# Kernel optimization log

Measured on AMD Instinct MI355X. Metric: run time of the kernel, lower is better.

Reference implementation:

```python
import jax, jax.numpy as jnp
import numpy as np

EMBED = 1024
HEADS = 16
HEAD_DIM = EMBED // HEADS
B, N = 2, 2048


def setup_inputs() -> dict:
    key = jax.random.key(0)
    ks = jax.random.split(key, 7)
    s = 1.0 / np.sqrt(EMBED)
    x = jax.random.normal(ks[0], (B, N, EMBED), dtype=jnp.float32)
    # causal mask: 1 where attention allowed, 0 elsewhere (masked_fill on mask==0)
    mask = jnp.tril(jnp.ones((N, N), dtype=jnp.int32))[None, None, :, :]
    Wq = jax.random.uniform(ks[1], (EMBED, EMBED), jnp.float32, -s, s)
    Wk = jax.random.uniform(ks[2], (EMBED, EMBED), jnp.float32, -s, s)
    Wv = jax.random.uniform(ks[3], (EMBED, EMBED), jnp.float32, -s, s)
    Wo = jax.random.uniform(ks[4], (EMBED, EMBED), jnp.float32, -s, s)
    bo = jax.random.uniform(ks[5], (EMBED,), jnp.float32, -s, s)
    return {"x": x, "mask": mask, "Wq": Wq, "Wk": Wk, "Wv": Wv, "Wo": Wo, "bo": bo}


def reference(x, mask, Wq, Wk, Wv, Wo, bo):
    Bx, Nx, D = x.shape
    # torch nn.Linear: y = x @ W.T
    q = (x @ Wq.T).reshape(Bx, Nx, HEADS, HEAD_DIM).transpose(0, 2, 1, 3)
    k = (x @ Wk.T).reshape(Bx, Nx, HEADS, HEAD_DIM).transpose(0, 2, 1, 3)
    v = (x @ Wv.T).reshape(Bx, Nx, HEADS, HEAD_DIM).transpose(0, 2, 1, 3)
    score = jnp.einsum('bhqd,bhkd->bhqk', q, k) / np.sqrt(HEAD_DIM).astype(np.float32)
    score = jnp.where(mask == 0, -jnp.inf, score)
    probs = jax.nn.softmax(score, axis=-1)
    out = jnp.einsum('bhqk,bhkd->bhqd', probs, v)  # [B,H,N,hd]
    out = out.transpose(0, 2, 1, 3).reshape(Bx, Nx, D)
    return out @ Wo.T + bo
```

## Files before the change

kernel.cpp:

```cpp
#include <hip/hip_runtime.h>
#include <hip/hip_bf16.h>

#define B_  2
#define N_  2048
#define E_  1024
#define H_  16
#define HD_ 64
#define M_  (B_*N_)
#define RSZ ((size_t)M_ * E_)

typedef short bf16x8 __attribute__((ext_vector_type(8)));
typedef float f32x4 __attribute__((ext_vector_type(4)));
typedef unsigned short u16x8 __attribute__((ext_vector_type(8)));

#define AS1 __attribute__((address_space(1)))
#define AS3 __attribute__((address_space(3)))

__device__ __forceinline__ unsigned short f2bfu(float f) {
    __hip_bfloat16 h = __float2bfloat16(f);
    return *reinterpret_cast<unsigned short*>(&h);
}
__device__ __forceinline__ unsigned int cvtpk(float lo, float hi) {
    unsigned int r;
    asm("v_cvt_pk_bf16_f32 %0, %1, %2" : "=v"(r) : "v"(lo), "v"(hi));
    return r;
}
#define MFMA16(a,b,c) __builtin_amdgcn_mfma_f32_16x16x32_bf16((a),(b),(c),0,0,0)

__device__ __forceinline__ void gl_lds16(const void* g, void* l) {
    __builtin_amdgcn_global_load_lds((const AS1 void*)g, (AS3 void*)l, 16, 0, 0);
}

__global__ __launch_bounds__(256) void fconv_all_kernel(
    const float* __restrict__ x,
    const float* __restrict__ Wq, const float* __restrict__ Wk,
    const float* __restrict__ Wv, const float* __restrict__ Wo,
    unsigned short* __restrict__ xbf, unsigned short* __restrict__ wbf)
{
    const int bid = blockIdx.x;
    const float* src;
    unsigned short* dst;
    int off;
    if (bid < 2048) {
        src = x; dst = xbf; off = bid * 2048 + threadIdx.x * 8;
    } else {
        const int z = (bid - 2048) >> 9;
        src = (z == 0) ? Wq : (z == 1 ? Wk : (z == 2 ? Wv : Wo));
        dst = wbf + (size_t)z * E_ * E_;
        off = ((bid - 2048) & 511) * 2048 + threadIdx.x * 8;
    }
    const float4 a = *reinterpret_cast<const float4*>(src + off);
    const float4 b = *reinterpret_cast<const float4*>(src + off + 4);
    u16x8 v;
    v[0]=f2bfu(a.x); v[1]=f2bfu(a.y); v[2]=f2bfu(a.z); v[3]=f2bfu(a.w);
    v[4]=f2bfu(b.x); v[5]=f2bfu(b.y); v[6]=f2bfu(b.z); v[7]=f2bfu(b.w);
    *reinterpret_cast<u16x8*>(dst + off) = v;
}

__global__ __launch_bounds__(256) void fconv_kernel(
    const float* __restrict__ src, unsigned short* __restrict__ dst)
{
    const int i0 = (blockIdx.x * 256 + threadIdx.x) * 8;
    const float4 a = *reinterpret_cast<const float4*>(src + i0);
    const float4 b = *reinterpret_cast<const float4*>(src + i0 + 4);
    u16x8 v;
    v[0]=f2bfu(a.x); v[1]=f2bfu(a.y); v[2]=f2bfu(a.z); v[3]=f2bfu(a.w);
    v[4]=f2bfu(b.x); v[5]=f2bfu(b.y); v[6]=f2bfu(b.z); v[7]=f2bfu(b.w);
    *reinterpret_cast<u16x8*>(dst + i0) = v;
}

__global__ __launch_bounds__(256) void qkv_fused_kernel(
    const unsigned short* __restrict__ xbf, const unsigned short* __restrict__ wbf,
    unsigned short* __restrict__ qkv)
{
    const int m0 = blockIdx.x * 64;
    const int n0 = blockIdx.y * 128;
    __shared__ unsigned short ldsA[64*64];
    __shared__ unsigned short ldsB[3][128*64];
    const int t = threadIdx.x;
    const int lane = t & 63;
    const int w = t >> 6, wr = w >> 1, wc = w & 1;
    const int fr = lane & 15, fq = lane >> 4;
    const int subrow = lane >> 3;
    const int csw = ((lane & 7) ^ subrow) * 8;
    const int rcol = ((fq * 8) ^ ((fr & 7) * 8));
    f32x4 acc[3][2][4] = {};

    for (int kt = 0; kt < 16; ++kt) {
        const int k0 = kt * 64;
        __syncthreads();
        #pragma unroll
        for (int i = 0; i < 14; ++i) {
            const int c = w * 14 + i;
            if (c < 8) {
                const int row = c * 8 + subrow;
                gl_lds16(xbf + (size_t)(m0 + row) * E_ + k0 + csw, &ldsA[c * 512]);
            } else {
                const int cc = c - 8;
                const int zb = cc >> 4, bc = cc & 15;
                const int row = bc * 8 + subrow;
                gl_lds16(wbf + (size_t)zb * E_ * E_ + (size_t)(n0 + row) * E_ + k0 + csw,
                         &ldsB[zb][bc * 512]);
            }
        }
        __syncthreads();
        #pragma unroll
        for (int ks = 0; ks < 2; ++ks) {
            bf16x8 af[2];
            #pragma unroll
            for (int mf = 0; mf < 2; ++mf)
                af[mf] = *(const bf16x8*)&ldsA[(wr*32 + mf*16 + fr)*64 + (rcol ^ (ks*32))];
            #pragma unroll
            for (int zb = 0; zb < 3; ++zb) {
                bf16x8 bfv[4];
                #pragma unroll
                for (int nf = 0; nf < 4; ++nf)
                    bfv[nf] = *(const bf16x8*)&ldsB[zb][(wc*64 + nf*16 + fr)*64 + (rcol ^ (ks*32))];
                #pragma unroll
                for (int mf = 0; mf < 2; ++mf)
                    #pragma unroll
                    for (int nf = 0; nf < 4; ++nf)
                        acc[zb][mf][nf] = MFMA16(af[mf], bfv[nf], acc[zb][mf][nf]);
            }
        }
    }

    #pragma unroll
    for (int zb = 0; zb < 3; ++zb) {
        unsigned short* __restrict__ out = qkv + (size_t)zb * RSZ;
        const float scale = (zb == 0) ? 0.125f : 1.0f;
        #pragma unroll
        for (int mf = 0; mf < 2; ++mf) {
            #pragma unroll
            for (int r = 0; r < 4; ++r) {
                const int m = m0 + wr*32 + mf*16 + fq*4 + r;
                const int b = m >> 11, npos = m & (N_ - 1);
                #pragma unroll
                for (int nf = 0; nf < 4; ++nf) {
                    const int n = n0 + wc*64 + nf*16 + fr;
                    const int h = n >> 6, d = n & 63;
                    const unsigned short val = f2bfu(acc[zb][mf][nf][r] * scale);
                    if (zb == 2)
                        out[(((size_t)(b*H_ + h))*HD_ + d)*N_ + npos] = val;
                    else
                        out[(((size_t)(b*H_ + h))*N_ + npos)*HD_ + d] = val;
                }
            }
        }
    }
}

__global__ __launch_bounds__(256) void qkv_f32_kernel(
    const float* __restrict__ x, const unsigned short* __restrict__ wbf,
    unsigned short* __restrict__ qkv)
{
    const int z = blockIdx.z;
    const unsigned short* __restrict__ W = wbf + (size_t)z * E_ * E_;
    unsigned short* __restrict__ out = qkv + (size_t)z * RSZ;
    const int m0 = blockIdx.x * 128;
    const int n0 = blockIdx.y * 128;
    __shared__ unsigned short As[128][72];
    __shared__ unsigned short Bs[128][72];
    const int t = threadIdx.x;
    const int lane = t & 63;
    const int w = t >> 6, wr = w >> 1, wc = w & 1;
    const int fr = lane & 15, fq = lane >> 4;
    const int srow = t >> 1, scol = (t & 1) * 32;
    f32x4 acc[4][4] = {};

    const float* arow = x + (size_t)(m0 + srow) * E_ + scol;
    const unsigned short* brow = W + (size_t)(n0 + srow) * E_ + scol;

    float4 a4[8];
    u16x8 b8[4];
    #pragma unroll
    for (int i = 0; i < 8; ++i) a4[i] = reinterpret_cast<const float4*>(arow)[i];
    #pragma unroll
    for (int i = 0; i < 4; ++i) b8[i] = reinterpret_cast<const u16x8*>(brow)[i];

    for (int k0 = 0; k0 < E_; k0 += 64) {
        __syncthreads();
        #pragma unroll
        for (int j = 0; j < 4; ++j) {
            u16x8 va;
            va[0]=f2bfu(a4[2*j].x); va[1]=f2bfu(a4[2*j].y); va[2]=f2bfu(a4[2*j].z); va[3]=f2bfu(a4[2*j].w);
            va[4]=f2bfu(a4[2*j+1].x); va[5]=f2bfu(a4[2*j+1].y); va[6]=f2bfu(a4[2*j+1].z); va[7]=f2bfu(a4[2*j+1].w);
            *reinterpret_cast<u16x8*>(&As[srow][scol + 8*j]) = va;
            *reinterpret_cast<u16x8*>(&Bs[srow][scol + 8*j]) = b8[j];
        }
        __syncthreads();
        if (k0 + 64 < E_) {
            #pragma unroll
            for (int i = 0; i < 8; ++i)
                a4[i] = reinterpret_cast<const float4*>(arow + k0 + 64)[i];
            #pragma unroll
            for (int i = 0; i < 4; ++i)
                b8[i] = reinterpret_cast<const u16x8*>(brow + k0 + 64)[i];
        }
        #pragma unroll
        for (int ks = 0; ks < 2; ++ks) {
            bf16x8 af[4], bfv[4];
            #pragma unroll
            for (int mf = 0; mf < 4; ++mf)
                af[mf] = *reinterpret_cast<const bf16x8*>(&As[wr*64 + mf*16 + fr][ks*32 + fq*8]);
            #pragma unroll
            for (int nf = 0; nf < 4; ++nf)
                bfv[nf] = *reinterpret_cast<const bf16x8*>(&Bs[wc*64 + nf*16 + fr][ks*32 + fq*8]);
            #pragma unroll
            for (int mf = 0; mf < 4; ++mf)
                #pragma unroll
                for (int nf = 0; nf < 4; ++nf)
                    acc[mf][nf] = MFMA16(af[mf], bfv[nf], acc[mf][nf]);
        }
    }

    const float scale = (z == 0) ? 0.125f : 1.0f;
    #pragma unroll
    for (int mf = 0; mf < 4; ++mf) {
        #pragma unroll
        for (int r = 0; r < 4; ++r) {
            const int m = m0 + wr*64 + mf*16 + fq*4 + r;
            const int b = m >> 11, npos = m & (N_ - 1);
            #pragma unroll
            for (int nf = 0; nf < 4; ++nf) {
                const int n = n0 + wc*64 + nf*16 + fr;
                const int h = n >> 6, d = n & 63;
                const unsigned short val = f2bfu(acc[mf][nf][r] * scale);
                if (z == 2)
                    out[(((size_t)(b*H_ + h))*HD_ + d)*N_ + npos] = val;
                else
                    out[(((size_t)(b*H_ + h))*N_ + npos)*HD_ + d] = val;
            }
        }
    }
}

__global__ __launch_bounds__(512) void attn_mfma_kernel(
    const unsigned short* __restrict__ qkv, unsigned short* __restrict__ attn_out)
{
    const int bh = blockIdx.x;
    const int xp = blockIdx.y;
    const unsigned short* Qp  = qkv + (size_t)bh * N_ * HD_;
    const unsigned short* Kp  = qkv + RSZ + (size_t)bh * N_ * HD_;
    const unsigned short* Vtp = qkv + 2*RSZ + (size_t)bh * N_ * HD_;
    __shared__ unsigned short Ks[128][72], Vt[64][136];
    const int t = threadIdx.x;
    const int lane = t & 63, w = t >> 6;
    const int fr = lane & 15, fq = lane >> 4;
    const int srK = t >> 2, scK = (t & 3) * 16;
    const int srV = t >> 3, scV = (t & 7) * 16;
    const int qbase = (w < 4) ? ((31 - xp) * 64 + w * 16)
                              : (xp * 64 + (w - 4) * 16);
    const int KT = (33 - xp) >> 1;
    const int ql = qbase + fr;
    const int lane_b0 = (2 * (fq & 1)) * 16 + fr;
    const int lane_b1 = lane_b0 + 16;
    const bool hi_sel = (fq >> 1) != 0;

    bf16x8 qfr[2];
    #pragma unroll
    for (int ks = 0; ks < 2; ++ks)
        qfr[ks] = *reinterpret_cast<const bf16x8*>(
            Qp + (size_t)ql * HD_ + ks*32 + fq*8);

    float m_run = -1e30f, l_run = 0.f;
    f32x4 o[4] = {};

    u16x8 kra = *reinterpret_cast<const u16x8*>(Kp + (size_t)srK * HD_ + scK);
    u16x8 krb = *reinterpret_cast<const u16x8*>(Kp + (size_t)srK * HD_ + scK + 8);
    u16x8 vra = *reinterpret_cast<const u16x8*>(Vtp + (size_t)srV * N_ + scV);
    u16x8 vrb = *reinterpret_cast<const u16x8*>(Vtp + (size_t)srV * N_ + scV + 8);

    for (int kt = 0; kt < KT; ++kt) {
        const int k0 = kt * 128;
        __syncthreads();
        *reinterpret_cast<u16x8*>(&Ks[srK][scK])     = kra;
        *reinterpret_cast<u16x8*>(&Ks[srK][scK + 8]) = krb;
        *reinterpret_cast<u16x8*>(&Vt[srV][scV])     = vra;
        *reinterpret_cast<u16x8*>(&Vt[srV][scV + 8]) = vrb;
        __syncthreads();
        if (kt + 1 < KT) {
            const int kn = k0 + 128;
            kra = *reinterpret_cast<const u16x8*>(Kp + (size_t)(kn + srK) * HD_ + scK);
            krb = *reinterpret_cast<const u16x8*>(Kp + (size_t)(kn + srK) * HD_ + scK + 8);
            vra = *reinterpret_cast<const u16x8*>(Vtp + (size_t)srV * N_ + kn + scV);
            vrb = *reinterpret_cast<const u16x8*>(Vtp + (size_t)srV * N_ + kn + scV + 8);
        }
        if (k0 > qbase + 15) continue;

        f32x4 s[8] = {};
        __builtin_amdgcn_s_setprio(1);
        #pragma unroll
        for (int ks = 0; ks < 2; ++ks) {
            #pragma unroll
            for (int nf = 0; nf < 8; ++nf) {
                bf16x8 bk = *reinterpret_cast<const bf16x8*>(&Ks[nf*16 + fr][ks*32 + fq*8]);
                s[nf] = MFMA16(bk, qfr[ks], s[nf]);
            }
        }
        __builtin_amdgcn_s_setprio(0);

        if (k0 + 127 > qbase) {
            #pragma unroll
            for (int nf = 0; nf < 8; ++nf)
                #pragma unroll
                for (int r = 0; r < 4; ++r)
                    if (k0 + nf*16 + fq*4 + r > ql) s[nf][r] = -1e30f;
        }

        float pm = -1e30f;
        #pragma unroll
        for (int nf = 0; nf < 8; ++nf)
            pm = fmaxf(pm, fmaxf(fmaxf(s[nf][0], s[nf][1]),
                                 fmaxf(s[nf][2], s[nf][3])));
        pm = fmaxf(pm, __shfl_xor(pm, 16));
        pm = fmaxf(pm, __shfl_xor(pm, 32));

        const bool need = __any(pm > m_run + 8.f);
        float scl = 1.f;
        if (need) {
            const float mnew = fmaxf(m_run, pm);
            scl = __expf(m_run - mnew);
            m_run = mnew;
        }

        float rs = 0.f;
        unsigned int u[8][2];
        #pragma unroll
        for (int nf = 0; nf < 8; ++nf) {
            const float p0 = __expf(s[nf][0] - m_run);
            const float p1 = __expf(s[nf][1] - m_run);
            const float p2 = __expf(s[nf][2] - m_run);
            const float p3 = __expf(s[nf][3] - m_run);
            rs += (p0 + p1) + (p2 + p3);
            u[nf][0] = cvtpk(p0, p1);
            u[nf][1] = cvtpk(p2, p3);
        }
        {
            float v = rs;
            v += __shfl_xor(v, 16);
            v += __shfl_xor(v, 32);
            l_run = l_run * scl + v;
        }
        if (need) {
            #pragma unroll
            for (int df = 0; df < 4; ++df)
                #pragma unroll
                for (int r = 0; r < 4; ++r)
                    o[df][r] *= scl;
        }

        bf16x8 pb[4];
        #pragma unroll
        for (int kk = 0; kk < 4; ++kk) {
            const unsigned int t00 = __shfl(u[2*kk+0][0], lane_b0);
            const unsigned int t01 = __shfl(u[2*kk+0][1], lane_b0);
            const unsigned int t02 = __shfl(u[2*kk+0][0], lane_b1);
            const unsigned int t03 = __shfl(u[2*kk+0][1], lane_b1);
            const unsigned int t10 = __shfl(u[2*kk+1][0], lane_b0);
            const unsigned int t11 = __shfl(u[2*kk+1][1], lane_b0);
            const unsigned int t12 = __shfl(u[2*kk+1][0], lane_b1);
            const unsigned int t13 = __shfl(u[2*kk+1][1], lane_b1);
            union { unsigned int wd[4]; bf16x8 v; } pu;
            pu.wd[0] = hi_sel ? t10 : t00;
            pu.wd[1] = hi_sel ? t11 : t01;
            pu.wd[2] = hi_sel ? t12 : t02;
            pu.wd[3] = hi_sel ? t13 : t03;
            pb[kk] = pu.v;
        }

        __builtin_amdgcn_s_setprio(1);
        #pragma unroll
        for (int kk = 0; kk < 4; ++kk) {
            bf16x8 bv[4];
            #pragma unroll
            for (int df = 0; df < 4; ++df)
                bv[df] = *reinterpret_cast<const bf16x8*>(&Vt[df*16 + fr][kk*32 + fq*8]);
            #pragma unroll
            for (int df = 0; df < 4; ++df)
                o[df] = MFMA16(bv[df], pb[kk], o[df]);
        }
        __builtin_amdgcn_s_setprio(0);
    }

    const int b = bh >> 4, h = bh & 15;
    const float inv = 1.0f / l_run;
    #pragma unroll
    for (int df = 0; df < 4; ++df)
        #pragma unroll
        for (int r = 0; r < 4; ++r) {
            const int d = df*16 + fq*4 + r;
            attn_out[((size_t)(b*N_ + ql))*E_ + h*64 + d] = f2bfu(o[df][r] * inv);
        }
}

__global__ __launch_bounds__(256) void out_glds_kernel(
    const unsigned short* __restrict__ A, const unsigned short* __restrict__ Wobf,
    const float* __restrict__ bo, float* __restrict__ out)
{
    const int m0 = blockIdx.x * 64;
    const int n0 = blockIdx.y * 128;
    __shared__ unsigned short ldsA[64*64];
    __shared__ unsigned short ldsB[128*64];
    const int t = threadIdx.x;
    const int lane = t & 63;
    const int w = t >> 6, wr = w >> 1, wc = w & 1;
    const int fr = lane & 15, fq = lane >> 4;
    const int subrow = lane >> 3;
    const int csw = ((lane & 7) ^ subrow) * 8;
    const int rcol = ((fq * 8) ^ ((fr & 7) * 8));
    f32x4 acc[2][4] = {};

    for (int kt = 0; kt < 16; ++kt) {
        const int k0 = kt * 64;
        __syncthreads();
        #pragma unroll
        for (int i = 0; i < 6; ++i) {
            const int c = w * 6 + i;
            if (c < 8) {
                const int row = c * 8 + subrow;
                gl_lds16(A + (size_t)(m0 + row) * E_ + k0 + csw, &ldsA[c * 512]);
            } else {
                const int row = (c - 8) * 8 + subrow;
                gl_lds16(Wobf + (size_t)(n0 + row) * E_ + k0 + csw, &ldsB[(c - 8) * 512]);
            }
        }
        __syncthreads();
        #pragma unroll
        for (int ks = 0; ks < 2; ++ks) {
            bf16x8 af[2], bfv[4];
            #pragma unroll
            for (int mf = 0; mf < 2; ++mf)
                af[mf] = *(const bf16x8*)&ldsA[(wr*32 + mf*16 + fr)*64 + (rcol ^ (ks*32))];
            #pragma unroll
            for (int nf = 0; nf < 4; ++nf)
                bfv[nf] = *(const bf16x8*)&ldsB[(wc*64 + nf*16 + fr)*64 + (rcol ^ (ks*32))];
            #pragma unroll
            for (int mf = 0; mf < 2; ++mf)
                #pragma unroll
                for (int nf = 0; nf < 4; ++nf)
                    acc[mf][nf] = MFMA16(af[mf], bfv[nf], acc[mf][nf]);
        }
    }

    #pragma unroll
    for (int mf = 0; mf < 2; ++mf) {
        #pragma unroll
        for (int r = 0; r < 4; ++r) {
            const int m = m0 + wr*32 + mf*16 + fq*4 + r;
            #pragma unroll
            for (int nf = 0; nf < 4; ++nf) {
                const int n = n0 + wc*64 + nf*16 + fr;
                out[(size_t)m * E_ + n] = acc[mf][nf][r] + bo[n];
            }
        }
    }
}

extern "C" void kernel_launch(void* const* d_in, const int* in_sizes, int n_in,
                              void* d_out, int out_size, void* d_ws, size_t ws_size,
                              hipStream_t stream) {
    const float* x  = (const float*)d_in[0];
    const float* Wq = (const float*)d_in[2];
    const float* Wk = (const float*)d_in[3];
    const float* Wv = (const float*)d_in[4];
    const float* Wo = (const float*)d_in[5];
    const float* bo = (const float*)d_in[6];
    float* out = (float*)d_out;

    unsigned short* ws = (unsigned short*)d_ws;
    const size_t need_main = 5 * RSZ * sizeof(unsigned short);

    if (ws_size >= need_main) {
        unsigned short* xbf  = ws;
        unsigned short* wbf  = ws + RSZ;
        unsigned short* qkvq = ws + 2 * RSZ;
        unsigned short* attn_ws = ws;
        unsigned short* wobf = wbf + 3 * (size_t)E_ * E_;

        fconv_all_kernel<<<4096, 256, 0, stream>>>(x, Wq, Wk, Wv, Wo, xbf, wbf);

        dim3 g1(M_ / 64, E_ / 128);
        qkv_fused_kernel<<<g1, 256, 0, stream>>>(xbf, wbf, qkvq);

        dim3 g2(B_ * H_, 16);
        attn_mfma_kernel<<<g2, 512, 0, stream>>>(qkvq, attn_ws);

        dim3 g3(M_ / 64, E_ / 128);
        out_glds_kernel<<<g3, 256, 0, stream>>>(attn_ws, wobf, bo, out);
    } else {
        unsigned short* wbf = ws;
        unsigned short* qkvq = ws + RSZ;
        unsigned short* attn_ws = ws;
        unsigned short* wobf = ws + RSZ;

        const int cgrid = E_ * E_ / (256 * 8);
        fconv_kernel<<<cgrid, 256, 0, stream>>>(Wq, wbf);
        fconv_kernel<<<cgrid, 256, 0, stream>>>(Wk, wbf + (size_t)E_ * E_);
        fconv_kernel<<<cgrid, 256, 0, stream>>>(Wv, wbf + 2 * (size_t)E_ * E_);

        dim3 g1(M_ / 128, E_ / 128, 3);
        qkv_f32_kernel<<<g1, 256, 0, stream>>>(x, wbf, qkvq);

        dim3 g2(B_ * H_, 16);
        attn_mfma_kernel<<<g2, 512, 0, stream>>>(qkvq, attn_ws);

        fconv_kernel<<<cgrid, 256, 0, stream>>>(Wo, wobf);

        dim3 g3(M_ / 64, E_ / 128);
        out_glds_kernel<<<g3, 256, 0, stream>>>(attn_ws, wobf, bo, out);
    }
}
```

Baseline: 105.9 us.

## Replace paired causal q-tiles with one q-tile per 256-thread block, heaviest first

The attention kernel previously paired a late and an early 64-row query tile in each 512-thread block so that causal work was balanced within the block. It now gives each 256-thread block a single 64-row query tile, launching twice as many blocks with the longest tiles scheduled first. Each thread stages twice as much K/V into shared memory per step. The aim is better occupancy and less K/V staging for early tiles, at the cost of relying on the hardware scheduler for load balance and more per-thread load registers.

```diff
diff --git a/kernel.cpp b/kernel.cpp
--- a/kernel.cpp
+++ b/kernel.cpp
@@ -235,11 +235,11 @@
     }
 }
 
-__global__ __launch_bounds__(512) void attn_mfma_kernel(
+__global__ __launch_bounds__(256) void attn_mfma_kernel(
     const unsigned short* __restrict__ qkv, unsigned short* __restrict__ attn_out)
 {
     const int bh = blockIdx.x;
-    const int xp = blockIdx.y;
+    const int qt = (int)(gridDim.y - 1) - (int)blockIdx.y;
     const unsigned short* Qp  = qkv + (size_t)bh * N_ * HD_;
     const unsigned short* Kp  = qkv + RSZ + (size_t)bh * N_ * HD_;
     const unsigned short* Vtp = qkv + 2*RSZ + (size_t)bh * N_ * HD_;
@@ -247,11 +247,10 @@
     const int t = threadIdx.x;
     const int lane = t & 63, w = t >> 6;
     const int fr = lane & 15, fq = lane >> 4;
-    const int srK = t >> 2, scK = (t & 3) * 16;
-    const int srV = t >> 3, scV = (t & 7) * 16;
-    const int qbase = (w < 4) ? ((31 - xp) * 64 + w * 16)
-                              : (xp * 64 + (w - 4) * 16);
-    const int KT = (33 - xp) >> 1;
+    const int srK = t >> 1, scK = (t & 1) * 32;
+    const int srV = t >> 2, scV = (t & 3) * 32;
+    const int qbase = qt * 64 + w * 16;
+    const int KT = (qt * 64 + 63) / 128 + 1;
     const int ql = qbase + fr;
     const int lane_b0 = (2 * (fq & 1)) * 16 + fr;
     const int lane_b1 = lane_b0 + 16;
@@ -266,25 +265,29 @@
     float m_run = -1e30f, l_run = 0.f;
     f32x4 o[4] = {};
 
-    u16x8 kra = *reinterpret_cast<const u16x8*>(Kp + (size_t)srK * HD_ + scK);
-    u16x8 krb = *reinterpret_cast<const u16x8*>(Kp + (size_t)srK * HD_ + scK + 8);
-    u16x8 vra = *reinterpret_cast<const u16x8*>(Vtp + (size_t)srV * N_ + scV);
-    u16x8 vrb = *reinterpret_cast<const u16x8*>(Vtp + (size_t)srV * N_ + scV + 8);
+    u16x8 kr[4], vr[4];
+    #pragma unroll
+    for (int j = 0; j < 4; ++j) {
+        kr[j] = *reinterpret_cast<const u16x8*>(Kp + (size_t)srK * HD_ + scK + 8*j);
+        vr[j] = *reinterpret_cast<const u16x8*>(Vtp + (size_t)srV * N_ + scV + 8*j);
+    }
 
     for (int kt = 0; kt < KT; ++kt) {
         const int k0 = kt * 128;
         __syncthreads();
-        *reinterpret_cast<u16x8*>(&Ks[srK][scK])     = kra;
-        *reinterpret_cast<u16x8*>(&Ks[srK][scK + 8]) = krb;
-        *reinterpret_cast<u16x8*>(&Vt[srV][scV])     = vra;
-        *reinterpret_cast<u16x8*>(&Vt[srV][scV + 8]) = vrb;
+        #pragma unroll
+        for (int j = 0; j < 4; ++j) {
+            *reinterpret_cast<u16x8*>(&Ks[srK][scK + 8*j]) = kr[j];
+            *reinterpret_cast<u16x8*>(&Vt[srV][scV + 8*j]) = vr[j];
+        }
         __syncthreads();
         if (kt + 1 < KT) {
             const int kn = k0 + 128;
-            kra = *reinterpret_cast<const u16x8*>(Kp + (size_t)(kn + srK) * HD_ + scK);
-            krb = *reinterpret_cast<const u16x8*>(Kp + (size_t)(kn + srK) * HD_ + scK + 8);
-            vra = *reinterpret_cast<const u16x8*>(Vtp + (size_t)srV * N_ + kn + scV);
-            vrb = *reinterpret_cast<const u16x8*>(Vtp + (size_t)srV * N_ + kn + scV + 8);
+            #pragma unroll
+            for (int j = 0; j < 4; ++j) {
+                kr[j] = *reinterpret_cast<const u16x8*>(Kp + (size_t)(kn + srK) * HD_ + scK + 8*j);
+                vr[j] = *reinterpret_cast<const u16x8*>(Vtp + (size_t)srV * N_ + kn + scV + 8*j);
+            }
         }
         if (k0 > qbase + 15) continue;
 
@@ -483,8 +486,8 @@
         dim3 g1(M_ / 64, E_ / 128);
         qkv_fused_kernel<<<g1, 256, 0, stream>>>(xbf, wbf, qkvq);
 
-        dim3 g2(B_ * H_, 16);
-        attn_mfma_kernel<<<g2, 512, 0, stream>>>(qkvq, attn_ws);
+        dim3 g2(B_ * H_, N_ / 64);
+        attn_mfma_kernel<<<g2, 256, 0, stream>>>(qkvq, attn_ws);
 
         dim3 g3(M_ / 64, E_ / 128);
         out_glds_kernel<<<g3, 256, 0, stream>>>(attn_ws, wobf, bo, out);
@@ -502,8 +505,8 @@
         dim3 g1(M_ / 128, E_ / 128, 3);
         qkv_f32_kernel<<<g1, 256, 0, stream>>>(x, wbf, qkvq);
 
-        dim3 g2(B_ * H_, 16);
-        attn_mfma_kernel<<<g2, 512, 0, stream>>>(qkvq, attn_ws);
+        dim3 g2(B_ * H_, N_ / 64);
+        attn_mfma_kernel<<<g2, 256, 0, stream>>>(qkvq, attn_ws);
 
         fconv_kernel<<<cgrid, 256, 0, stream>>>(Wo, wobf);
 
```

Result: slower. 109.9 us (+3.8%).
